# Kernel optimization log

Hardware: AMD Instinct MI355X
Metric: run time of the kernel (lower is better)

## Reference

```python
import jax, jax.numpy as jnp
import numpy as np

B, T, D = 4, 2048, 1024

def setup_inputs() -> dict:
    key = jax.random.key(0)
    kx, kq, kk, kv = jax.random.split(key, 4)
    scale = 1.0 / np.sqrt(D)
    return {
        "x": jax.random.normal(kx, (B, T, D), dtype=jnp.float32),
        "Wq": jax.random.normal(kq, (D, D), dtype=jnp.float32) * scale,
        "Wk": jax.random.normal(kk, (D, D), dtype=jnp.float32) * scale,
        "Wv": jax.random.normal(kv, (D, D), dtype=jnp.float32) * scale,
    }

def reference(x, Wq, Wk, Wv):
    # torch Linear: y = x @ W.T (no bias, qkv_bias=False)
    q = jnp.einsum("btd,od->bto", x, Wq)
    k = jnp.einsum("btd,od->bto", x, Wk)
    v = jnp.einsum("btd,od->bto", x, Wv)
    scores = jnp.einsum("bqd,bkd->bqk", q, k)
    # NOTE: source uses non-in-place masked_fill whose result is discarded,
    # so NO causal mask is actually applied. Faithfully reproduced here.
    inv_sqrt_d = 1.0 / np.sqrt(k.shape[-1]).astype(np.float32)
    weights = jax.nn.softmax(scores * inv_sqrt_d, axis=-1)
    # dropout p=0.0 -> identity
    return jnp.einsum("bqk,bkd->bqd", weights, v)
```

## Files before the change

### kernel.cpp

```cpp
#include <hip/hip_runtime.h>
#include <hip/hip_bf16.h>
#include <hip/hip_fp16.h>
#include <type_traits>

typedef _Float16 f16;
typedef __attribute__((ext_vector_type(8))) _Float16 f16x8;
typedef __attribute__((ext_vector_type(4))) float floatx4;

#define B_ 4
#define T_ 2048
#define D_ 1024

#define XB_OFF   0ul
#define WB_OFF   16777216ul
#define QKV_OFF  23068672ul
#define S_OFF    73400320ul
#define VT_OFF   0ul

#define ASYNC16(gp, lp) \
    __builtin_amdgcn_global_load_lds((const __attribute__((address_space(1))) unsigned int*)(gp), \
                                     (__attribute__((address_space(3))) unsigned int*)(lp), 16, 0, 0)

__global__ __launch_bounds__(256) void cast_all(
    const float* __restrict__ x, const float* __restrict__ wq,
    const float* __restrict__ wk, const float* __restrict__ wv,
    f16* __restrict__ xb, f16* __restrict__ wb)
{
    long i = (long)blockIdx.x * 256 + threadIdx.x;
    const float4* src; f16* dst;
    if (i < 2097152L)            { src = (const float4*)x;  dst = xb; }
    else if (i < 2359296L)       { i -= 2097152L; src = (const float4*)wq; dst = wb; }
    else if (i < 2621440L)       { i -= 2359296L; src = (const float4*)wk; dst = wb + 1048576; }
    else                         { i -= 2621440L; src = (const float4*)wv; dst = wb + 2097152; }
    float4 v = src[i];
    union { f16 h[4]; uint2 u; } o;
    o.h[0] = (f16)v.x; o.h[1] = (f16)v.y; o.h[2] = (f16)v.z; o.h[3] = (f16)v.w;
    ((uint2*)dst)[i] = o.u;
}

template <typename CT>
__global__ __launch_bounds__(256) void gemm_nt(
    const f16* __restrict__ A, int lda, long sA,
    const f16* __restrict__ B, int ldb, long sB,
    CT* __restrict__ C, int ldc, long sC,
    int K, float alpha)
{
    __shared__ f16 As[128 * 32];
    __shared__ f16 Bs[128 * 32];

    const int tid = threadIdx.x;
    const int m0 = blockIdx.y * 128;
    const int n0 = blockIdx.x * 128;
    const int bz = blockIdx.z;
    A += (long)bz * sA;
    B += (long)bz * sB;
    C += (long)bz * sC;

    const int w  = tid >> 6;
    const int l  = tid & 63;
    const int wm = (w >> 1) * 64;
    const int wn = (w & 1) * 64;
    const int lr = l & 15;
    const int kg = l >> 4;

    const int srow = tid >> 2;
    const int scol = (tid & 3) * 8;

    floatx4 acc[4][4] = {};

    const long ldaL = lda, ldbL = ldb;
    const f16* Aptr = A + (long)(m0 + srow) * ldaL + scol;
    const f16* Bptr = B + (long)(n0 + srow) * ldbL + scol;
    f16* AsW = &As[w * 512];
    f16* BsW = &Bs[w * 512];

    for (int k0 = 0; k0 < K; k0 += 32) {
        ASYNC16(Aptr,             AsW);
        ASYNC16(Aptr + 64 * ldaL, AsW + 64 * 32);
        ASYNC16(Bptr,             BsW);
        ASYNC16(Bptr + 64 * ldbL, BsW + 64 * 32);
        __syncthreads();

        f16x8 af[4], bf[4];
        #pragma unroll
        for (int mi = 0; mi < 4; mi++)
            af[mi] = *(const f16x8*)&As[(wm + mi * 16 + lr) * 32 + kg * 8];
        #pragma unroll
        for (int ni = 0; ni < 4; ni++)
            bf[ni] = *(const f16x8*)&Bs[(wn + ni * 16 + lr) * 32 + kg * 8];
        #pragma unroll
        for (int mi = 0; mi < 4; mi++)
            #pragma unroll
            for (int ni = 0; ni < 4; ni++)
                acc[mi][ni] = __builtin_amdgcn_mfma_f32_16x16x32_f16(af[mi], bf[ni], acc[mi][ni], 0, 0, 0);

        __syncthreads();
        Aptr += 32; Bptr += 32;
    }

    #pragma unroll
    for (int mi = 0; mi < 4; mi++) {
        #pragma unroll
        for (int ni = 0; ni < 4; ni++) {
            #pragma unroll
            for (int r = 0; r < 4; r++) {
                int row = m0 + wm + mi * 16 + kg * 4 + r;
                int col = n0 + wn + ni * 16 + lr;
                float v = acc[mi][ni][r] * alpha;
                if constexpr (std::is_same<CT, float>::value)
                    C[(long)row * ldc + col] = v;
                else
                    C[(long)row * ldc + col] = (f16)v;
            }
        }
    }
}

__global__ __launch_bounds__(256) void transpose_v(const f16* __restrict__ qkv, f16* __restrict__ vt)
{
    __shared__ f16 tile[32][33];
    int b  = blockIdx.z;
    int j0 = blockIdx.x * 32;
    int d0 = blockIdx.y * 32;
    int tx = threadIdx.x & 31;
    int ty = threadIdx.x >> 5;
    #pragma unroll
    for (int i = 0; i < 4; i++) {
        int j = j0 + ty + i * 8;
        tile[ty + i * 8][tx] = qkv[((long)b * T_ + j) * 3072 + 2048 + d0 + tx];
    }
    __syncthreads();
    #pragma unroll
    for (int i = 0; i < 4; i++) {
        int d = d0 + ty + i * 8;
        vt[((long)b * D_ + d) * T_ + j0 + tx] = tile[tx][ty + i * 8];
    }
}

__global__ __launch_bounds__(256) void softmax_rows(f16* __restrict__ S)
{
    long row = blockIdx.x;
    f16* p = S + row * 2048;
    union { uint4 u; f16 h[8]; } d;
    d.u = ((const uint4*)p)[threadIdx.x];
    float v[8];
    float mx = -1e30f;
    #pragma unroll
    for (int i = 0; i < 8; i++) { v[i] = (float)d.h[i]; mx = fmaxf(mx, v[i]); }
    #pragma unroll
    for (int off = 32; off; off >>= 1) mx = fmaxf(mx, __shfl_xor(mx, off, 64));
    __shared__ float redm[4];
    __shared__ float reds[4];
    int w = threadIdx.x >> 6, l = threadIdx.x & 63;
    if (l == 0) redm[w] = mx;
    __syncthreads();
    mx = fmaxf(fmaxf(redm[0], redm[1]), fmaxf(redm[2], redm[3]));
    float s = 0.f;
    #pragma unroll
    for (int i = 0; i < 8; i++) { v[i] = __expf(v[i] - mx); s += v[i]; }
    #pragma unroll
    for (int off = 32; off; off >>= 1) s += __shfl_xor(s, off, 64);
    if (l == 0) reds[w] = s;
    __syncthreads();
    s = reds[0] + reds[1] + reds[2] + reds[3];
    float inv = 1.f / s;
    #pragma unroll
    for (int i = 0; i < 8; i++) d.h[i] = (f16)(v[i] * inv);
    ((uint4*)p)[threadIdx.x] = d.u;
}

extern "C" void kernel_launch(void* const* d_in, const int* in_sizes, int n_in,
                              void* d_out, int out_size, void* d_ws, size_t ws_size,
                              hipStream_t stream)
{
    const float* x  = (const float*)d_in[0];
    const float* wq = (const float*)d_in[1];
    const float* wk = (const float*)d_in[2];
    const float* wv = (const float*)d_in[3];
    float* out = (float*)d_out;
    char* ws = (char*)d_ws;
    f16* xb  = (f16*)(ws + XB_OFF);
    f16* wb  = (f16*)(ws + WB_OFF);
    f16* qkv = (f16*)(ws + QKV_OFF);
    f16* s   = (f16*)(ws + S_OFF);
    f16* vt  = (f16*)(ws + VT_OFF);

    cast_all<<<11264, 256, 0, stream>>>(x, wq, wk, wv, xb, wb);

    gemm_nt<f16><<<dim3(24, 64, 1), 256, 0, stream>>>(
        xb, 1024, 0L, wb, 1024, 0L, qkv, 3072, 0L, 1024, 1.0f);

    transpose_v<<<dim3(64, 32, 4), 256, 0, stream>>>(qkv, vt);

    gemm_nt<f16><<<dim3(16, 16, 4), 256, 0, stream>>>(
        qkv,        3072, (long)T_ * 3072,
        qkv + 1024, 3072, (long)T_ * 3072,
        s,          2048, (long)T_ * 2048, 1024, 0.03125f);

    softmax_rows<<<8192, 256, 0, stream>>>(s);

    gemm_nt<float><<<dim3(8, 16, 4), 256, 0, stream>>>(
        s,  2048, (long)T_ * 2048,
        vt, 2048, (long)D_ * 2048,
        out, 1024, (long)T_ * 1024, 2048, 1.0f);
}
```

Baseline: 306.8 us.

## Restructure GEMM LDS layout to k-slab major, BK=64, templated BN; wave-per-row softmax

```diff
diff --git a/kernel.cpp b/kernel.cpp
--- a/kernel.cpp
+++ b/kernel.cpp
@@ -38,70 +38,82 @@
     ((uint2*)dst)[i] = o.u;
 }
 
-template <typename CT>
+template <typename CT, int BN>
 __global__ __launch_bounds__(256) void gemm_nt(
     const f16* __restrict__ A, int lda, long sA,
     const f16* __restrict__ B, int ldb, long sB,
     CT* __restrict__ C, int ldc, long sC,
     int K, float alpha)
 {
-    __shared__ f16 As[128 * 32];
-    __shared__ f16 Bs[128 * 32];
+    __shared__ f16 As[8 * 128 * 8];
+    __shared__ f16 Bs[8 * BN * 8];
 
     const int tid = threadIdx.x;
     const int m0 = blockIdx.y * 128;
-    const int n0 = blockIdx.x * 128;
+    const int n0 = blockIdx.x * BN;
     const int bz = blockIdx.z;
-    A += (long)bz * sA;
-    B += (long)bz * sB;
+    A += (long)bz * sA + (long)m0 * lda;
+    B += (long)bz * sB + (long)n0 * ldb;
     C += (long)bz * sC;
 
     const int w  = tid >> 6;
     const int l  = tid & 63;
     const int wm = (w >> 1) * 64;
-    const int wn = (w & 1) * 64;
+    const int wn = (w & 1) * (BN / 2);
     const int lr = l & 15;
     const int kg = l >> 4;
 
-    const int srow = tid >> 2;
-    const int scol = (tid & 3) * 8;
-
-    floatx4 acc[4][4] = {};
-
-    const long ldaL = lda, ldbL = ldb;
-    const f16* Aptr = A + (long)(m0 + srow) * ldaL + scol;
-    const f16* Bptr = B + (long)(n0 + srow) * ldbL + scol;
-    f16* AsW = &As[w * 512];
-    f16* BsW = &Bs[w * 512];
-
-    for (int k0 = 0; k0 < K; k0 += 32) {
-        ASYNC16(Aptr,             AsW);
-        ASYNC16(Aptr + 64 * ldaL, AsW + 64 * 32);
-        ASYNC16(Bptr,             BsW);
-        ASYNC16(Bptr + 64 * ldbL, BsW + 64 * 32);
+    constexpr int NI = BN / 32;
+    floatx4 acc[4][NI] = {};
+
+    const f16* Al = A + (long)l * lda;
+    const f16* Bl = B + (long)l * ldb;
+
+    for (int k0 = 0; k0 < K; k0 += 64) {
+        #pragma unroll
+        for (int c = 0; c < 4; c++) {
+            int ks = 2 * w + (c >> 1);
+            int rh = c & 1;
+            ASYNC16(Al + k0 + ks * 8 + rh * 64 * lda, &As[ks * 1024 + rh * 512]);
+        }
+        if constexpr (BN == 128) {
+            #pragma unroll
+            for (int c = 0; c < 4; c++) {
+                int ks = 2 * w + (c >> 1);
+                int rh = c & 1;
+                ASYNC16(Bl + k0 + ks * 8 + rh * 64 * ldb, &Bs[ks * 1024 + rh * 512]);
+            }
+        } else {
+            #pragma unroll
+            for (int c = 0; c < 2; c++) {
+                int ks = 2 * w + c;
+                ASYNC16(Bl + k0 + ks * 8, &Bs[ks * 512]);
+            }
+        }
         __syncthreads();
 
-        f16x8 af[4], bf[4];
-        #pragma unroll
-        for (int mi = 0; mi < 4; mi++)
-            af[mi] = *(const f16x8*)&As[(wm + mi * 16 + lr) * 32 + kg * 8];
-        #pragma unroll
-        for (int ni = 0; ni < 4; ni++)
-            bf[ni] = *(const f16x8*)&Bs[(wn + ni * 16 + lr) * 32 + kg * 8];
-        #pragma unroll
-        for (int mi = 0; mi < 4; mi++)
-            #pragma unroll
-            for (int ni = 0; ni < 4; ni++)
-                acc[mi][ni] = __builtin_amdgcn_mfma_f32_16x16x32_f16(af[mi], bf[ni], acc[mi][ni], 0, 0, 0);
-
+        #pragma unroll
+        for (int s = 0; s < 2; s++) {
+            f16x8 af[4], bf[NI];
+            #pragma unroll
+            for (int mi = 0; mi < 4; mi++)
+                af[mi] = *(const f16x8*)&As[(s * 4 + kg) * 1024 + (wm + mi * 16 + lr) * 8];
+            #pragma unroll
+            for (int ni = 0; ni < NI; ni++)
+                bf[ni] = *(const f16x8*)&Bs[(s * 4 + kg) * (BN * 8) + (wn + ni * 16 + lr) * 8];
+            #pragma unroll
+            for (int mi = 0; mi < 4; mi++)
+                #pragma unroll
+                for (int ni = 0; ni < NI; ni++)
+                    acc[mi][ni] = __builtin_amdgcn_mfma_f32_16x16x32_f16(af[mi], bf[ni], acc[mi][ni], 0, 0, 0);
+        }
         __syncthreads();
-        Aptr += 32; Bptr += 32;
     }
 
     #pragma unroll
     for (int mi = 0; mi < 4; mi++) {
         #pragma unroll
-        for (int ni = 0; ni < 4; ni++) {
+        for (int ni = 0; ni < NI; ni++) {
             #pragma unroll
             for (int r = 0; r < 4; r++) {
                 int row = m0 + wm + mi * 16 + kg * 4 + r;
@@ -139,34 +151,32 @@
 
 __global__ __launch_bounds__(256) void softmax_rows(f16* __restrict__ S)
 {
-    long row = blockIdx.x;
-    f16* p = S + row * 2048;
-    union { uint4 u; f16 h[8]; } d;
-    d.u = ((const uint4*)p)[threadIdx.x];
-    float v[8];
+    long row = (long)blockIdx.x * 4 + (threadIdx.x >> 6);
+    int l = threadIdx.x & 63;
+    uint4* p4 = (uint4*)(S + row * 2048);
+    union U { uint4 u; f16 h[8]; } d[4];
+    float v[32];
     float mx = -1e30f;
     #pragma unroll
-    for (int i = 0; i < 8; i++) { v[i] = (float)d.h[i]; mx = fmaxf(mx, v[i]); }
+    for (int i = 0; i < 4; i++) {
+        d[i].u = p4[i * 64 + l];
+        #pragma unroll
+        for (int j = 0; j < 8; j++) { v[i * 8 + j] = (float)d[i].h[j]; mx = fmaxf(mx, v[i * 8 + j]); }
+    }
     #pragma unroll
     for (int off = 32; off; off >>= 1) mx = fmaxf(mx, __shfl_xor(mx, off, 64));
-    __shared__ float redm[4];
-    __shared__ float reds[4];
-    int w = threadIdx.x >> 6, l = threadIdx.x & 63;
-    if (l == 0) redm[w] = mx;
-    __syncthreads();
-    mx = fmaxf(fmaxf(redm[0], redm[1]), fmaxf(redm[2], redm[3]));
     float s = 0.f;
     #pragma unroll
-    for (int i = 0; i < 8; i++) { v[i] = __expf(v[i] - mx); s += v[i]; }
+    for (int i = 0; i < 32; i++) { v[i] = __expf(v[i] - mx); s += v[i]; }
     #pragma unroll
     for (int off = 32; off; off >>= 1) s += __shfl_xor(s, off, 64);
-    if (l == 0) reds[w] = s;
-    __syncthreads();
-    s = reds[0] + reds[1] + reds[2] + reds[3];
     float inv = 1.f / s;
     #pragma unroll
-    for (int i = 0; i < 8; i++) d.h[i] = (f16)(v[i] * inv);
-    ((uint4*)p)[threadIdx.x] = d.u;
+    for (int i = 0; i < 4; i++) {
+        #pragma unroll
+        for (int j = 0; j < 8; j++) d[i].h[j] = (f16)(v[i * 8 + j] * inv);
+        p4[i * 64 + l] = d[i].u;
+    }
 }
 
 extern "C" void kernel_launch(void* const* d_in, const int* in_sizes, int n_in,
@@ -187,19 +197,19 @@
 
     cast_all<<<11264, 256, 0, stream>>>(x, wq, wk, wv, xb, wb);
 
-    gemm_nt<f16><<<dim3(24, 64, 1), 256, 0, stream>>>(
+    gemm_nt<f16, 128><<<dim3(24, 64, 1), 256, 0, stream>>>(
         xb, 1024, 0L, wb, 1024, 0L, qkv, 3072, 0L, 1024, 1.0f);
 
     transpose_v<<<dim3(64, 32, 4), 256, 0, stream>>>(qkv, vt);
 
-    gemm_nt<f16><<<dim3(16, 16, 4), 256, 0, stream>>>(
+    gemm_nt<f16, 128><<<dim3(16, 16, 4), 256, 0, stream>>>(
         qkv,        3072, (long)T_ * 3072,
         qkv + 1024, 3072, (long)T_ * 3072,
         s,          2048, (long)T_ * 2048, 1024, 0.03125f);
 
-    softmax_rows<<<8192, 256, 0, stream>>>(s);
-
-    gemm_nt<float><<<dim3(8, 16, 4), 256, 0, stream>>>(
+    softmax_rows<<<2048, 256, 0, stream>>>(s);
+
+    gemm_nt<float, 64><<<dim3(16, 16, 4), 256, 0, stream>>>(
         s,  2048, (long)T_ * 2048,
         vt, 2048, (long)D_ * 2048,
         out, 1024, (long)T_ * 1024, 2048, 1.0f);
```

Measured after the change: 390.2 us. +27.2%, slower.
